# Kernel tuning notes

Hardware: AMD Instinct MI355X
Metric: run time of the kernel (lower is better)

The kernel has to match this reference:

```python
import jax, jax.numpy as jnp
import numpy as np

B = 128
K = 16
# (in_ch, featdim, dim) per stage, matching conv1..conv11
DIMS = [(3, 8, 2048), (8, 32, 1024), (32, 64, 512), (64, 64, 256), (64, 64, 128),
        (64, 128, 64), (128, 256, 32), (256, 512, 16), (512, 512, 8), (512, 512, 4),
        (512, 1024, 2)]


def setup_inputs() -> dict:
    key = jax.random.key(0)
    ks = jax.random.split(key, 64)
    inp = {"x": jax.random.normal(ks[0], (B, 3, 2048), dtype=jnp.float32)}
    i = 1
    for li, (cin, cf, d) in enumerate(DIMS, start=1):
        inp[f"W{li}"] = jax.random.normal(ks[i], (3 * cf, cin), dtype=jnp.float32) / np.sqrt(cin).astype(np.float32); i += 1
        inp[f"b{li}"] = jax.random.normal(ks[i], (3 * cf,), dtype=jnp.float32) * 0.01; i += 1
        inp[f"sel{li}"] = jax.random.randint(ks[i], (d,), 0, 3); i += 1
    inp["fcW"] = jax.random.normal(ks[i], (K, 1024), dtype=jnp.float32) / np.sqrt(1024).astype(np.float32); i += 1
    inp["fcb"] = jax.random.normal(ks[i], (K,), dtype=jnp.float32) * 0.01
    return inp


def kdconv(x, W, b, sel, featdim, dim):
    # 1x1 conv == per-position matmul: x [B, Cin, dim] -> y [B, 3*featdim, dim]
    y = jax.nn.relu(jnp.einsum('oi,bin->bon', W, x) + b[None, :, None])
    y = y.reshape(-1, featdim, 3, dim)
    # kd split-dim gather: pick one of the 3 feature groups per position
    y = jnp.take_along_axis(y, sel[None, None, None, :], axis=2)[:, :, 0, :]  # [B, featdim, dim]
    # pairwise max-pool of sibling leaves
    return y.reshape(-1, featdim, dim // 2, 2).max(axis=-1)  # [B, featdim, dim//2]


def reference(x, sel1, sel2, sel3, sel4, sel5, sel6, sel7, sel8, sel9, sel10, sel11,
              W1, b1, W2, b2, W3, b3, W4, b4, W5, b5, W6, b6, W7, b7, W8, b8,
              W9, b9, W10, b10, W11, b11, fcW, fcb):
    Ws = [W1, W2, W3, W4, W5, W6, W7, W8, W9, W10, W11]
    bs = [b1, b2, b3, b4, b5, b6, b7, b8, b9, b10, b11]
    sels = [sel1, sel2, sel3, sel4, sel5, sel6, sel7, sel8, sel9, sel10, sel11]
    h = x
    for (cin, cf, d), W, b, s in zip(DIMS, Ws, bs, sels):
        h = kdconv(h, W, b, s, cf, d)
    h = h.reshape(-1, 1024)  # [B, 1024]
    return jax.nn.log_softmax(h @ fcW.T + fcb, axis=-1)
```

## Files before the change

kernel.cpp:

```cpp
#include <hip/hip_runtime.h>
#include <math.h>

typedef __attribute__((ext_vector_type(8))) short bf16x8;
typedef __attribute__((ext_vector_type(4))) float f32x4;

__device__ __forceinline__ unsigned short f2bf(float f) {
    unsigned u = __builtin_bit_cast(unsigned, f);
    u += 0x7FFF + ((u >> 16) & 1);
    return (unsigned short)(u >> 16);
}
__device__ __forceinline__ float bf2f(unsigned short h) {
    unsigned u = ((unsigned)h) << 16;
    return __builtin_bit_cast(float, u);
}

#define O_W8 153600
#define O_W9 546816
#define O_W10 1333248
#define O_W11 2119680

__device__ __forceinline__ bf16x8 ldcvt8(const float* p) {
    float4 u0 = *(const float4*)p;
    float4 u1 = *(const float4*)(p + 4);
    bf16x8 r;
    r[0] = (short)f2bf(u0.x); r[1] = (short)f2bf(u0.y);
    r[2] = (short)f2bf(u0.z); r[3] = (short)f2bf(u0.w);
    r[4] = (short)f2bf(u1.x); r[5] = (short)f2bf(u1.y);
    r[6] = (short)f2bf(u1.z); r[7] = (short)f2bf(u1.w);
    return r;
}

template<int CIN>
__device__ __forceinline__ void mfma_tile_f32A(
    const float* a0f, const float* a1f,
    const unsigned short* b0p, const unsigned short* b1p,
    f32x4& acc0, f32x4& acc1)
{
#pragma unroll
    for (int k = 0; k < CIN; k += 32) {
        bf16x8 A0 = ldcvt8(a0f + k);
        bf16x8 A1 = ldcvt8(a1f + k);
        bf16x8 B0 = __builtin_bit_cast(bf16x8, *(const float4*)(const void*)(b0p + k));
        bf16x8 B1 = __builtin_bit_cast(bf16x8, *(const float4*)(const void*)(b1p + k));
        acc0 = __builtin_amdgcn_mfma_f32_16x16x32_bf16(A0, B0, acc0, 0, 0, 0);
        acc1 = __builtin_amdgcn_mfma_f32_16x16x32_bf16(A1, B1, acc1, 0, 0, 0);
    }
}

__device__ __forceinline__ void epilogue_store(
    unsigned short* dst, const f32x4& acc0, const f32x4& acc1,
    const float* bias, int fbase, int s0, int s1)
{
    unsigned short o[4];
#pragma unroll
    for (int r = 0; r < 4; ++r) {
        float v = fmaxf(fmaxf(acc0[r] + bias[(fbase + r) * 3 + s0],
                              acc1[r] + bias[(fbase + r) * 3 + s1]), 0.f);
        o[r] = f2bf(v);
    }
    *(ushort4*)dst = make_ushort4(o[0], o[1], o[2], o[3]);
}

struct KAParams {
    const float* x;
    const float* W1; const float* B1; const int* S1;
    const float* W2; const float* B2; const int* S2;
    const float* Wsrc[9];
    unsigned short* Wb;
    unsigned short* X3;
};

__global__ __launch_bounds__(256) void ka_l12_pack(KAParams P)
{
    const int tid = threadIdx.x;

    if (blockIdx.x >= 128) {
        int gt = (blockIdx.x - 128) * 256 + tid;
        const int we[4] = {393216, 786432, 786432, 1572864};
        const int wo[4] = {O_W8, O_W9, O_W10, O_W11};
#pragma unroll
        for (int li = 0; li < 4; ++li) {
            const float4* src = (const float4*)P.Wsrc[5 + li];
            ushort4* dst = (ushort4*)(P.Wb + wo[li]);
            int n4 = we[li] >> 2;
            for (int i = gt; i < n4; i += 32768) {
                float4 w = src[i];
                dst[i] = make_ushort4(f2bf(w.x), f2bf(w.y), f2bf(w.z), f2bf(w.w));
            }
        }
        return;
    }

    __shared__ __align__(16) float xsf[16 * 396];
    __shared__ float wsm[960];
    __shared__ unsigned short L1o[64 * 16 * 8];
    __shared__ int selA[192];

    const int bg = blockIdx.x >> 4;
    const int sl = blockIdx.x & 15;

    {
        const float* xg = P.x + (size_t)(bg * 16) * 6144 + sl * 128;
        for (int i = tid; i < 6144; i += 256) {
            int b = i / 384;
            int r = i - b * 384;
            int cc = r >> 7, p = r & 127;
            xsf[b * 396 + cc * 132 + p] = xg[(size_t)b * 6144 + cc * 2048 + p];
        }
        if (tid < 72)            wsm[tid] = P.W1[tid];
        else if (tid < 96)       wsm[tid] = P.B1[tid - 72];
        for (int i = tid; i < 768; i += 256) wsm[96 + i] = P.W2[i];
        if (tid < 96)            wsm[864 + tid] = P.B2[tid];
        if (tid < 128)           selA[tid] = P.S1[sl * 128 + tid];
        else if (tid < 192)      selA[tid] = P.S2[sl * 64 + (tid - 128)];
    }
    __syncthreads();

    {
        const float* wl1 = wsm;
        const float* bl1 = wsm + 72;
        for (int i = tid; i < 1024; i += 256) {
            int n = i >> 4, b = i & 15;
            int s0 = selA[2 * n], s1 = selA[2 * n + 1];
            const float* xb0 = xsf + b * 396 + 2 * n;
            float c0x = xb0[0],   c0y = xb0[1];
            float c1x = xb0[132], c1y = xb0[133];
            float c2x = xb0[264], c2y = xb0[265];
            unsigned short o[8];
#pragma unroll
            for (int f = 0; f < 8; ++f) {
                int r0 = f * 3 + s0, r1 = f * 3 + s1;
                float z0 = fmaf(wl1[r0*3+2], c2x, fmaf(wl1[r0*3+1], c1x, fmaf(wl1[r0*3+0], c0x, bl1[r0])));
                float z1 = fmaf(wl1[r1*3+2], c2y, fmaf(wl1[r1*3+1], c1y, fmaf(wl1[r1*3+0], c0y, bl1[r1])));
                o[f] = f2bf(fmaxf(fmaxf(z0, z1), 0.f));
            }
            unsigned short* dst = L1o + (n * 16 + b) * 8;
            *(ushort4*)dst       = make_ushort4(o[0], o[1], o[2], o[3]);
            *(ushort4*)(dst + 4) = make_ushort4(o[4], o[5], o[6], o[7]);
        }
    }
    __syncthreads();

    {
        const float* wl2 = wsm + 96;
        const float* bl2 = wsm + 864;
        for (int i = tid; i < 1024; i += 256) {
            int n = i >> 5, b = (i >> 1) & 15, fh = i & 1;
            int s0 = selA[128 + 2 * n], s1 = selA[128 + 2 * n + 1];
            const unsigned short* r0 = L1o + ((2 * n) * 16 + b) * 8;
            const unsigned short* r1 = L1o + ((2 * n + 1) * 16 + b) * 8;
            float xa[8], xb2[8];
            {
                ushort4 u0 = *(const ushort4*)r0, u1 = *(const ushort4*)(r0 + 4);
                ushort4 v0 = *(const ushort4*)r1, v1 = *(const ushort4*)(r1 + 4);
                xa[0]=bf2f(u0.x); xa[1]=bf2f(u0.y); xa[2]=bf2f(u0.z); xa[3]=bf2f(u0.w);
                xa[4]=bf2f(u1.x); xa[5]=bf2f(u1.y); xa[6]=bf2f(u1.z); xa[7]=bf2f(u1.w);
                xb2[0]=bf2f(v0.x); xb2[1]=bf2f(v0.y); xb2[2]=bf2f(v0.z); xb2[3]=bf2f(v0.w);
                xb2[4]=bf2f(v1.x); xb2[5]=bf2f(v1.y); xb2[6]=bf2f(v1.z); xb2[7]=bf2f(v1.w);
            }
            unsigned short o[16];
#pragma unroll
            for (int fl = 0; fl < 16; ++fl) {
                int f = fh * 16 + fl;
                const float* w0 = &wl2[(f * 3 + s0) * 8];
                const float* w1 = &wl2[(f * 3 + s1) * 8];
                float z0 = bl2[f * 3 + s0], z1 = bl2[f * 3 + s1];
#pragma unroll
                for (int k = 0; k < 8; ++k) {
                    z0 = fmaf(w0[k], xa[k], z0);
                    z1 = fmaf(w1[k], xb2[k], z1);
                }
                o[fl] = f2bf(fmaxf(fmaxf(z0, z1), 0.f));
            }
            unsigned short* dst = P.X3 + ((size_t)(sl * 32 + n) * 128 + bg * 16 + b) * 32 + fh * 16;
#pragma unroll
            for (int i2 = 0; i2 < 4; ++i2)
                *(ushort4*)(dst + 4 * i2) = make_ushort4(o[4*i2], o[4*i2+1], o[4*i2+2], o[4*i2+3]);
        }
    }
}

struct KBParams {
    const float* Wsrc[9];
    const float* Bl[9];
    const int*   Sl[9];
    const unsigned short* X3;
    unsigned short* X8;
};

#define B_SELB 0
#define B_L3O  8192
#define B_L4O  45056
#define B_L5O  8192
#define B_L6O  45056
#define B_ARENA 63488

__global__ __launch_bounds__(512) void kb_l37(KBParams P)
{
    __shared__ __align__(16) char arena[B_ARENA];

    const int tid  = threadIdx.x;
    const int bg   = blockIdx.x >> 4;
    const int sl   = blockIdx.x & 15;
    const int lane = tid & 63;
    const int wv   = tid >> 6;
    const int c    = lane & 15, q = lane >> 4;

    int*   si  = (int*)(arena + B_SELB);
    float* bfs = (float*)(arena + B_SELB + 1024);
    const int* S3L = si;
    const int* S4L = si + 32;
    const int* S5L = si + 48;
    const int* S6L = si + 56;
    const int* S7L = si + 60;
    const float* B3L = bfs;
    const float* B4L = bfs + 192;
    const float* B5L = bfs + 384;
    const float* B6L = bfs + 576;
    const float* B7L = bfs + 960;

    if (tid < 32)       si[tid] = P.Sl[0][sl * 32 + tid];
    else if (tid < 48)  si[tid] = P.Sl[1][sl * 16 + (tid - 32)];
    else if (tid < 56)  si[tid] = P.Sl[2][sl * 8 + (tid - 48)];
    else if (tid < 60)  si[tid] = P.Sl[3][sl * 4 + (tid - 56)];
    else if (tid < 62)  si[tid] = P.Sl[4][sl * 2 + (tid - 60)];
    for (int i = tid; i < 1728; i += 512) {
        float v;
        if (i < 192)      v = P.Bl[0][i];
        else if (i < 384) v = P.Bl[1][i - 192];
        else if (i < 576) v = P.Bl[2][i - 384];
        else if (i < 960) v = P.Bl[3][i - 576];
        else              v = P.Bl[4][i - 960];
        bfs[i] = v;
    }
    __syncthreads();

    {
        unsigned short* L3o = (unsigned short*)(arena + B_L3O);
        const float* W3f = P.Wsrc[0];
#pragma unroll 2
        for (int t = wv; t < 64; t += 8) {
            int n3 = t >> 2, ft = t & 3;
            int s0 = __builtin_amdgcn_readfirstlane(S3L[2 * n3]);
            int s1 = __builtin_amdgcn_readfirstlane(S3L[2 * n3 + 1]);
            int f0 = ft * 16;
            const float* a0f = W3f + ((f0 + c) * 3 + s0) * 32 + q * 8;
            const float* a1f = W3f + ((f0 + c) * 3 + s1) * 32 + q * 8;
            const unsigned short* bp0 = P.X3 + ((size_t)(sl * 32 + 2 * n3) * 128 + bg * 16 + c) * 32 + q * 8;
            const unsigned short* bp1 = P.X3 + ((size_t)(sl * 32 + 2 * n3 + 1) * 128 + bg * 16 + c) * 32 + q * 8;
            f32x4 acc0 = {0.f,0.f,0.f,0.f}, acc1 = {0.f,0.f,0.f,0.f};
            mfma_tile_f32A<32>(a0f, a1f, bp0, bp1, acc0, acc1);
            epilogue_store(L3o + (n3 * 16 + c) * 72 + f0 + q * 4,
                           acc0, acc1, B3L, f0 + q * 4, s0, s1);
        }
    }
    __syncthreads();

    {
        const unsigned short* L3o = (const unsigned short*)(arena + B_L3O);
        unsigned short* L4o = (unsigned short*)(arena + B_L4O);
        const float* W4f = P.Wsrc[1];
#pragma unroll 2
        for (int t = wv; t < 32; t += 8) {
            int n4 = t >> 2, ft = t & 3;
            int s0 = __builtin_amdgcn_readfirstlane(S4L[2 * n4]);
            int s1 = __builtin_amdgcn_readfirstlane(S4L[2 * n4 + 1]);
            int f0 = ft * 16;
            const float* a0f = W4f + ((f0 + c) * 3 + s0) * 64 + q * 8;
            const float* a1f = W4f + ((f0 + c) * 3 + s1) * 64 + q * 8;
            const unsigned short* bp0 = L3o + ((2 * n4) * 16 + c) * 72 + q * 8;
            const unsigned short* bp1 = L3o + ((2 * n4 + 1) * 16 + c) * 72 + q * 8;
            f32x4 acc0 = {0.f,0.f,0.f,0.f}, acc1 = {0.f,0.f,0.f,0.f};
            mfma_tile_f32A<64>(a0f, a1f, bp0, bp1, acc0, acc1);
            epilogue_store(L4o + (n4 * 16 + c) * 72 + f0 + q * 4,
                           acc0, acc1, B4L, f0 + q * 4, s0, s1);
        }
    }
    __syncthreads();

    {
        const unsigned short* L4o = (const unsigned short*)(arena + B_L4O);
        unsigned short* L5o = (unsigned short*)(arena + B_L5O);
        const float* W5f = P.Wsrc[2];
#pragma unroll
        for (int t = wv; t < 16; t += 8) {
            int n5 = t >> 2, ft = t & 3;
            int s0 = __builtin_amdgcn_readfirstlane(S5L[2 * n5]);
            int s1 = __builtin_amdgcn_readfirstlane(S5L[2 * n5 + 1]);
            int f0 = ft * 16;
            const float* a0f = W5f + ((f0 + c) * 3 + s0) * 64 + q * 8;
            const float* a1f = W5f + ((f0 + c) * 3 + s1) * 64 + q * 8;
            const unsigned short* bp0 = L4o + ((2 * n5) * 16 + c) * 72 + q * 8;
            const unsigned short* bp1 = L4o + ((2 * n5 + 1) * 16 + c) * 72 + q * 8;
            f32x4 acc0 = {0.f,0.f,0.f,0.f}, acc1 = {0.f,0.f,0.f,0.f};
            mfma_tile_f32A<64>(a0f, a1f, bp0, bp1, acc0, acc1);
            epilogue_store(L5o + (n5 * 16 + c) * 72 + f0 + q * 4,
                           acc0, acc1, B5L, f0 + q * 4, s0, s1);
        }
    }
    __syncthreads();

    {
        const unsigned short* L5o = (const unsigned short*)(arena + B_L5O);
        unsigned short* L6o = (unsigned short*)(arena + B_L6O);
        const float* W6f = P.Wsrc[3];
#pragma unroll
        for (int t = wv; t < 16; t += 8) {
            int n6 = t >> 3, ft = t & 7;
            int s0 = __builtin_amdgcn_readfirstlane(S6L[2 * n6]);
            int s1 = __builtin_amdgcn_readfirstlane(S6L[2 * n6 + 1]);
            int f0 = ft * 16;
            const float* a0f = W6f + ((f0 + c) * 3 + s0) * 64 + q * 8;
            const float* a1f = W6f + ((f0 + c) * 3 + s1) * 64 + q * 8;
            const unsigned short* bp0 = L5o + ((2 * n6) * 16 + c) * 72 + q * 8;
            const unsigned short* bp1 = L5o + ((2 * n6 + 1) * 16 + c) * 72 + q * 8;
            f32x4 acc0 = {0.f,0.f,0.f,0.f}, acc1 = {0.f,0.f,0.f,0.f};
            mfma_tile_f32A<64>(a0f, a1f, bp0, bp1, acc0, acc1);
            epilogue_store(L6o + (n6 * 16 + c) * 136 + f0 + q * 4,
                           acc0, acc1, B6L, f0 + q * 4, s0, s1);
        }
    }
    __syncthreads();

    {
        const unsigned short* L6o = (const unsigned short*)(arena + B_L6O);
        const float* W7f = P.Wsrc[4];
        int s0 = __builtin_amdgcn_readfirstlane(S7L[0]);
        int s1 = __builtin_amdgcn_readfirstlane(S7L[1]);
#pragma unroll
        for (int t = wv; t < 16; t += 8) {
            int f0 = t * 16;
            const float* a0f = W7f + (size_t)((f0 + c) * 3 + s0) * 128 + q * 8;
            const float* a1f = W7f + (size_t)((f0 + c) * 3 + s1) * 128 + q * 8;
            const unsigned short* bp0 = L6o + (0 * 16 + c) * 136 + q * 8;
            const unsigned short* bp1 = L6o + (1 * 16 + c) * 136 + q * 8;
            f32x4 acc0 = {0.f,0.f,0.f,0.f}, acc1 = {0.f,0.f,0.f,0.f};
            mfma_tile_f32A<128>(a0f, a1f, bp0, bp1, acc0, acc1);
            epilogue_store(P.X8 + ((size_t)sl * 128 + bg * 16 + c) * 256 + f0 + q * 4,
                           acc0, acc1, B7L, f0 + q * 4, s0, s1);
        }
    }
}

template<int CIN, int CF, int NP, int MW, int NW>
__global__ __launch_bounds__(256) void mfma_kernel(
    const unsigned short* __restrict__ Xin,
    const unsigned short* __restrict__ Wb,
    const float* __restrict__ bias,
    const int*   __restrict__ sel,
    unsigned short* __restrict__ Xout)
{
    constexpr int FT = CF / (16 * MW);
    constexpr int BT = 128 / (16 * NW);

    const int wid  = threadIdx.x >> 6;
    const int lane = threadIdx.x & 63;
    const int task = blockIdx.x * 4 + wid;
    const int bi = task % BT;
    const int fi = (task / BT) % FT;
    const int n  = task / (BT * FT);

    const int c = lane & 15;
    const int q = lane >> 4;
    const int s0 = __builtin_amdgcn_readfirstlane(sel[2 * n]);
    const int s1 = __builtin_amdgcn_readfirstlane(sel[2 * n + 1]);

    const int f0 = fi * 16 * MW;
    const int b0 = bi * 16 * NW;

    const unsigned short* ap[2][MW];
    const unsigned short* bp[2][NW];
#pragma unroll
    for (int p = 0; p < 2; ++p) {
        int s = p ? s1 : s0;
#pragma unroll
        for (int mi = 0; mi < MW; ++mi)
            ap[p][mi] = Wb + (size_t)((f0 + mi * 16 + c) * 3 + s) * CIN + q * 8;
#pragma unroll
        for (int ni = 0; ni < NW; ++ni)
            bp[p][ni] = Xin + ((size_t)(2 * n + p) * 128 + b0 + ni * 16 + c) * CIN + q * 8;
    }

    f32x4 acc[2][MW][NW];
#pragma unroll
    for (int p = 0; p < 2; ++p)
#pragma unroll
        for (int mi = 0; mi < MW; ++mi)
#pragma unroll
            for (int ni = 0; ni < NW; ++ni)
                acc[p][mi][ni] = (f32x4){0.f, 0.f, 0.f, 0.f};

#pragma unroll 2
    for (int k = 0; k < CIN; k += 32) {
        bf16x8 A[2][MW], B[2][NW];
#pragma unroll
        for (int p = 0; p < 2; ++p) {
#pragma unroll
            for (int mi = 0; mi < MW; ++mi)
                A[p][mi] = __builtin_bit_cast(bf16x8, *(const float4*)(const void*)(ap[p][mi] + k));
#pragma unroll
            for (int ni = 0; ni < NW; ++ni)
                B[p][ni] = __builtin_bit_cast(bf16x8, *(const float4*)(const void*)(bp[p][ni] + k));
        }
#pragma unroll
        for (int p = 0; p < 2; ++p)
#pragma unroll
            for (int mi = 0; mi < MW; ++mi)
#pragma unroll
                for (int ni = 0; ni < NW; ++ni)
                    acc[p][mi][ni] = __builtin_amdgcn_mfma_f32_16x16x32_bf16(
                        A[p][mi], B[p][ni], acc[p][mi][ni], 0, 0, 0);
    }

#pragma unroll
    for (int mi = 0; mi < MW; ++mi) {
        int fbase = f0 + mi * 16 + q * 4;
#pragma unroll
        for (int ni = 0; ni < NW; ++ni) {
            int b = b0 + ni * 16 + c;
            epilogue_store(Xout + ((size_t)n * 128 + b) * CF + fbase,
                           acc[0][mi][ni], acc[1][mi][ni], bias, fbase, s0, s1);
        }
    }
}

__global__ __launch_bounds__(256) void fc_logsoftmax_kernel(
    const unsigned short* __restrict__ h, const float* __restrict__ fcW,
    const float* __restrict__ fcb, float* __restrict__ out)
{
    int b   = blockIdx.x;
    int tid = threadIdx.x;
    int k     = tid & 15;
    int chunk = tid >> 4;

    const float* __restrict__ wk = fcW + (size_t)k * 1024;
    const unsigned short* hb = h + (size_t)b * 1024;

    float partial = 0.0f;
    int j0 = chunk * 64;
#pragma unroll 8
    for (int j = 0; j < 64; ++j)
        partial = fmaf(bf2f(hb[j0 + j]), wk[j0 + j], partial);

    __shared__ float red[16][17];
    red[chunk][k] = partial;
    __syncthreads();

    __shared__ float logits[16];
    if (tid < 16) {
        float s = fcb[tid];
#pragma unroll
        for (int c = 0; c < 16; ++c) s += red[c][tid];
        logits[tid] = s;
    }
    __syncthreads();

    if (tid < 16) {
        float mx = -INFINITY;
#pragma unroll
        for (int kk = 0; kk < 16; ++kk) mx = fmaxf(mx, logits[kk]);
        float se = 0.0f;
#pragma unroll
        for (int kk = 0; kk < 16; ++kk) se += expf(logits[kk] - mx);
        out[b * 16 + tid] = logits[tid] - mx - logf(se);
    }
}

extern "C" void kernel_launch(void* const* d_in, const int* in_sizes, int n_in,
                              void* d_out, int out_size, void* d_ws, size_t ws_size,
                              hipStream_t stream)
{
#define WL(i) (const float*)d_in[1 + 3 * (i)]
#define BL(i) (const float*)d_in[2 + 3 * (i)]
#define SL(i) (const int*)  d_in[3 + 3 * (i)]

    unsigned short* bufA = (unsigned short*)d_ws;
    unsigned short* bufB = bufA + 2u * 1024u * 1024u;
    unsigned short* X3   = bufB + 2u * 1024u * 1024u;
    unsigned short* Wb   = X3   + 2u * 1024u * 1024u;

    KAParams KA;
    KA.x  = (const float*)d_in[0];
    KA.W1 = WL(0); KA.B1 = BL(0); KA.S1 = SL(0);
    KA.W2 = WL(1); KA.B2 = BL(1); KA.S2 = SL(1);
    for (int i = 0; i < 9; ++i) KA.Wsrc[i] = WL(2 + i);
    KA.Wb = Wb; KA.X3 = X3;
    ka_l12_pack<<<256, 256, 0, stream>>>(KA);

    KBParams KB;
    for (int i = 0; i < 9; ++i) {
        KB.Wsrc[i] = WL(2 + i);
        KB.Bl[i]   = BL(2 + i);
        KB.Sl[i]   = SL(2 + i);
    }
    KB.X3 = X3; KB.X8 = bufA;
    kb_l37<<<128, 512, 0, stream>>>(KB);

    mfma_kernel<256, 512, 8, 2, 2><<<128, 256, 0, stream>>>(bufA, Wb + O_W8,  BL(7),  SL(7),  bufB);
    mfma_kernel<512, 512, 4, 1, 1><<<256, 256, 0, stream>>>(bufB, Wb + O_W9,  BL(8),  SL(8),  bufA);
    mfma_kernel<512, 512, 2, 1, 1><<<128, 256, 0, stream>>>(bufA, Wb + O_W10, BL(9),  SL(9),  bufB);
    mfma_kernel<512, 1024, 1, 1, 1><<<128, 256, 0, stream>>>(bufB, Wb + O_W11, BL(10), SL(10), bufA);

    fc_logsoftmax_kernel<<<128, 256, 0, stream>>>(bufA, (const float*)d_in[34], (const float*)d_in[35], (float*)d_out);

#undef WL
#undef BL
#undef SL
}
```

Measured before the change: 220.8 us.

## Compute layers 1-2 per lane in registers and prefetch early weights into cache

Layers 1 and 2 are rewritten so each lane loads its four input positions directly from global memory with vector loads and computes the full 32-channel output. This removes the shared-memory staging of x, the intermediate L1 buffer and a barrier. The grid doubles to 512 blocks, 256 for compute and 256 for the bf16 weight packing. The pack blocks also read the layer 3-7 weights into a discarded sum to warm the cache for the next kernel. In exchange there are more registers per thread and extra redundant global reads.

```diff
diff --git a/kernel.cpp b/kernel.cpp
--- a/kernel.cpp
+++ b/kernel.cpp
@@ -61,7 +61,7 @@
     *(ushort4*)dst = make_ushort4(o[0], o[1], o[2], o[3]);
 }
 
-struct KAParams {
+struct HeadParams {
     const float* x;
     const float* W1; const float* B1; const int* S1;
     const float* W2; const float* B2; const int* S2;
@@ -70,12 +70,12 @@
     unsigned short* X3;
 };
 
-__global__ __launch_bounds__(256) void ka_l12_pack(KAParams P)
+__global__ __launch_bounds__(256) void head_l12_pack(HeadParams P)
 {
     const int tid = threadIdx.x;
 
-    if (blockIdx.x >= 128) {
-        int gt = (blockIdx.x - 128) * 256 + tid;
+    if (blockIdx.x >= 256) {
+        int gt = (blockIdx.x - 256) * 256 + tid;
         const int we[4] = {393216, 786432, 786432, 1572864};
         const int wo[4] = {O_W8, O_W9, O_W10, O_W11};
 #pragma unroll
@@ -83,101 +83,97 @@
             const float4* src = (const float4*)P.Wsrc[5 + li];
             ushort4* dst = (ushort4*)(P.Wb + wo[li]);
             int n4 = we[li] >> 2;
-            for (int i = gt; i < n4; i += 32768) {
+            for (int i = gt; i < n4; i += 65536) {
                 float4 w = src[i];
                 dst[i] = make_ushort4(f2bf(w.x), f2bf(w.y), f2bf(w.z), f2bf(w.w));
             }
         }
+        float4 acc = {0.f, 0.f, 0.f, 0.f};
+        const int wn[5] = {6144, 12288, 12288, 24576, 98304};
+#pragma unroll
+        for (int li = 0; li < 5; ++li) {
+            const float4* src = (const float4*)P.Wsrc[li];
+            int n4 = wn[li] >> 2;
+            for (int i = gt; i < n4; i += 65536) {
+                float4 v = src[i];
+                acc.x += v.x; acc.y += v.y; acc.z += v.z; acc.w += v.w;
+            }
+        }
+        float s = acc.x + acc.y + acc.z + acc.w;
+        asm volatile("" :: "v"(s));
         return;
     }
 
-    __shared__ __align__(16) float xsf[16 * 396];
     __shared__ float wsm[960];
-    __shared__ unsigned short L1o[64 * 16 * 8];
-    __shared__ int selA[192];
-
-    const int bg = blockIdx.x >> 4;
-    const int sl = blockIdx.x & 15;
-
-    {
-        const float* xg = P.x + (size_t)(bg * 16) * 6144 + sl * 128;
-        for (int i = tid; i < 6144; i += 256) {
-            int b = i / 384;
-            int r = i - b * 384;
-            int cc = r >> 7, p = r & 127;
-            xsf[b * 396 + cc * 132 + p] = xg[(size_t)b * 6144 + cc * 2048 + p];
-        }
-        if (tid < 72)            wsm[tid] = P.W1[tid];
-        else if (tid < 96)       wsm[tid] = P.B1[tid - 72];
-        for (int i = tid; i < 768; i += 256) wsm[96 + i] = P.W2[i];
-        if (tid < 96)            wsm[864 + tid] = P.B2[tid];
-        if (tid < 128)           selA[tid] = P.S1[sl * 128 + tid];
-        else if (tid < 192)      selA[tid] = P.S2[sl * 64 + (tid - 128)];
-    }
-    __syncthreads();
-
-    {
-        const float* wl1 = wsm;
-        const float* bl1 = wsm + 72;
-        for (int i = tid; i < 1024; i += 256) {
-            int n = i >> 4, b = i & 15;
-            int s0 = selA[2 * n], s1 = selA[2 * n + 1];
-            const float* xb0 = xsf + b * 396 + 2 * n;
-            float c0x = xb0[0],   c0y = xb0[1];
-            float c1x = xb0[132], c1y = xb0[133];
-            float c2x = xb0[264], c2y = xb0[265];
-            unsigned short o[8];
-#pragma unroll
-            for (int f = 0; f < 8; ++f) {
-                int r0 = f * 3 + s0, r1 = f * 3 + s1;
-                float z0 = fmaf(wl1[r0*3+2], c2x, fmaf(wl1[r0*3+1], c1x, fmaf(wl1[r0*3+0], c0x, bl1[r0])));
-                float z1 = fmaf(wl1[r1*3+2], c2y, fmaf(wl1[r1*3+1], c1y, fmaf(wl1[r1*3+0], c0y, bl1[r1])));
-                o[f] = f2bf(fmaxf(fmaxf(z0, z1), 0.f));
+    for (int i = tid; i < 960; i += 256) {
+        float v;
+        if (i < 72)       v = P.W1[i];
+        else if (i < 96)  v = P.B1[i - 72];
+        else if (i < 864) v = P.W2[i - 96];
+        else              v = P.B2[i - 864];
+        wsm[i] = v;
+    }
+    __syncthreads();
+
+    const float* wl1 = wsm;
+    const float* bl1 = wsm + 72;
+    const float* wl2 = wsm + 96;
+    const float* bl2 = wsm + 864;
+
+    const int lane = tid & 63;
+    const int gw   = blockIdx.x * 4 + (tid >> 6);
+    const int b    = gw >> 3;
+    const int chunk= gw & 7;
+    const int np2  = chunk * 64 + lane;
+
+    const float* xb = P.x + (size_t)b * 6144 + chunk * 256 + 4 * lane;
+    float4 x0 = *(const float4*)(xb);
+    float4 x1 = *(const float4*)(xb + 2048);
+    float4 x2 = *(const float4*)(xb + 4096);
+    int4 sA = *(const int4*)(P.S1 + 4 * np2);
+    int2 sB = *(const int2*)(P.S2 + 2 * np2);
+
+    float y1a[8], y1b[8];
+    {
+        int s0 = sA.x, s1 = sA.y;
+#pragma unroll
+        for (int f = 0; f < 8; ++f) {
+            int r0 = f * 3 + s0, r1 = f * 3 + s1;
+            float z0 = fmaf(wl1[r0*3+2], x2.x, fmaf(wl1[r0*3+1], x1.x, fmaf(wl1[r0*3+0], x0.x, bl1[r0])));
+            float z1 = fmaf(wl1[r1*3+2], x2.y, fmaf(wl1[r1*3+1], x1.y, fmaf(wl1[r1*3+0], x0.y, bl1[r1])));
+            y1a[f] = bf2f(f2bf(fmaxf(fmaxf(z0, z1), 0.f)));
+        }
+        int t0 = sA.z, t1 = sA.w;
+#pragma unroll
+        for (int f = 0; f < 8; ++f) {
+            int r0 = f * 3 + t0, r1 = f * 3 + t1;
+            float z0 = fmaf(wl1[r0*3+2], x2.z, fmaf(wl1[r0*3+1], x1.z, fmaf(wl1[r0*3+0], x0.z, bl1[r0])));
+            float z1 = fmaf(wl1[r1*3+2], x2.w, fmaf(wl1[r1*3+1], x1.w, fmaf(wl1[r1*3+0], x0.w, bl1[r1])));
+            y1b[f] = bf2f(f2bf(fmaxf(fmaxf(z0, z1), 0.f)));
+        }
+    }
+
+    unsigned short o[32];
+    {
+        int s0 = sB.x, s1 = sB.y;
+#pragma unroll
+        for (int f = 0; f < 32; ++f) {
+            const float* w0 = &wl2[(f * 3 + s0) * 8];
+            const float* w1 = &wl2[(f * 3 + s1) * 8];
+            float z0 = bl2[f * 3 + s0], z1 = bl2[f * 3 + s1];
+#pragma unroll
+            for (int k = 0; k < 8; ++k) {
+                z0 = fmaf(w0[k], y1a[k], z0);
+                z1 = fmaf(w1[k], y1b[k], z1);
             }
-            unsigned short* dst = L1o + (n * 16 + b) * 8;
-            *(ushort4*)dst       = make_ushort4(o[0], o[1], o[2], o[3]);
-            *(ushort4*)(dst + 4) = make_ushort4(o[4], o[5], o[6], o[7]);
-        }
-    }
-    __syncthreads();
-
-    {
-        const float* wl2 = wsm + 96;
-        const float* bl2 = wsm + 864;
-        for (int i = tid; i < 1024; i += 256) {
-            int n = i >> 5, b = (i >> 1) & 15, fh = i & 1;
-            int s0 = selA[128 + 2 * n], s1 = selA[128 + 2 * n + 1];
-            const unsigned short* r0 = L1o + ((2 * n) * 16 + b) * 8;
-            const unsigned short* r1 = L1o + ((2 * n + 1) * 16 + b) * 8;
-            float xa[8], xb2[8];
-            {
-                ushort4 u0 = *(const ushort4*)r0, u1 = *(const ushort4*)(r0 + 4);
-                ushort4 v0 = *(const ushort4*)r1, v1 = *(const ushort4*)(r1 + 4);
-                xa[0]=bf2f(u0.x); xa[1]=bf2f(u0.y); xa[2]=bf2f(u0.z); xa[3]=bf2f(u0.w);
-                xa[4]=bf2f(u1.x); xa[5]=bf2f(u1.y); xa[6]=bf2f(u1.z); xa[7]=bf2f(u1.w);
-                xb2[0]=bf2f(v0.x); xb2[1]=bf2f(v0.y); xb2[2]=bf2f(v0.z); xb2[3]=bf2f(v0.w);
-                xb2[4]=bf2f(v1.x); xb2[5]=bf2f(v1.y); xb2[6]=bf2f(v1.z); xb2[7]=bf2f(v1.w);
-            }
-            unsigned short o[16];
-#pragma unroll
-            for (int fl = 0; fl < 16; ++fl) {
-                int f = fh * 16 + fl;
-                const float* w0 = &wl2[(f * 3 + s0) * 8];
-                const float* w1 = &wl2[(f * 3 + s1) * 8];
-                float z0 = bl2[f * 3 + s0], z1 = bl2[f * 3 + s1];
-#pragma unroll
-                for (int k = 0; k < 8; ++k) {
-                    z0 = fmaf(w0[k], xa[k], z0);
-                    z1 = fmaf(w1[k], xb2[k], z1);
-                }
-                o[fl] = f2bf(fmaxf(fmaxf(z0, z1), 0.f));
-            }
-            unsigned short* dst = P.X3 + ((size_t)(sl * 32 + n) * 128 + bg * 16 + b) * 32 + fh * 16;
-#pragma unroll
-            for (int i2 = 0; i2 < 4; ++i2)
-                *(ushort4*)(dst + 4 * i2) = make_ushort4(o[4*i2], o[4*i2+1], o[4*i2+2], o[4*i2+3]);
-        }
-    }
+            o[f] = f2bf(fmaxf(fmaxf(z0, z1), 0.f));
+        }
+    }
+
+    unsigned short* dst = P.X3 + ((size_t)np2 * 128 + b) * 32;
+#pragma unroll
+    for (int i2 = 0; i2 < 8; ++i2)
+        *(ushort4*)(dst + 4 * i2) = make_ushort4(o[4*i2], o[4*i2+1], o[4*i2+2], o[4*i2+3]);
 }
 
 struct KBParams {
@@ -479,13 +475,13 @@
     unsigned short* X3   = bufB + 2u * 1024u * 1024u;
     unsigned short* Wb   = X3   + 2u * 1024u * 1024u;
 
-    KAParams KA;
-    KA.x  = (const float*)d_in[0];
-    KA.W1 = WL(0); KA.B1 = BL(0); KA.S1 = SL(0);
-    KA.W2 = WL(1); KA.B2 = BL(1); KA.S2 = SL(1);
-    for (int i = 0; i < 9; ++i) KA.Wsrc[i] = WL(2 + i);
-    KA.Wb = Wb; KA.X3 = X3;
-    ka_l12_pack<<<256, 256, 0, stream>>>(KA);
+    HeadParams HP;
+    HP.x  = (const float*)d_in[0];
+    HP.W1 = WL(0); HP.B1 = BL(0); HP.S1 = SL(0);
+    HP.W2 = WL(1); HP.B2 = BL(1); HP.S2 = SL(1);
+    for (int i = 0; i < 9; ++i) HP.Wsrc[i] = WL(2 + i);
+    HP.Wb = Wb; HP.X3 = X3;
+    head_l12_pack<<<512, 256, 0, stream>>>(HP);
 
     KBParams KB;
     for (int i = 0; i < 9; ++i) {
```

After: 216.3 us. 2.1% less time.
